# Kernel tuning notes

Hardware: AMD Instinct MI355X
Metric: run time of the kernel (lower is better)

The kernel has to match this reference:

```python
import jax, jax.numpy as jnp
import numpy as np

B = 262144
G = 21       # number of groups (hardcoded in the torch forward)
GS = 8       # features per group
BASIC = 13   # data[:, :13]
H = 512      # hidden_dim
OUT = 1      # output_size


def setup_inputs() -> dict:
    key = jax.random.key(0)
    k0, k1, k2, k3, k4, k5, k6 = jax.random.split(key, 7)
    data = jax.random.normal(k0, (B, BASIC + G * GS), dtype=jnp.float32)
    # per-group Linear(GS, 1): stacked weights [G, GS] and biases [G]
    gW = jax.random.normal(k1, (G, GS), dtype=jnp.float32) * 0.1
    gb = jax.random.normal(k2, (G,), dtype=jnp.float32) * 0.1
    W1 = jax.random.normal(k3, (BASIC + G, H), dtype=jnp.float32) * 0.1
    b1 = jax.random.normal(k4, (H,), dtype=jnp.float32) * 0.1
    W2 = jax.random.normal(k5, (H, OUT), dtype=jnp.float32) * 0.1
    b2 = jax.random.normal(k6, (OUT,), dtype=jnp.float32) * 0.1
    return {"data": data, "gW": gW, "gb": gb, "W1": W1, "b1": b1, "W2": W2, "b2": b2}


def reference(data, gW, gb, W1, b1, W2, b2):
    # Groups are the contiguous, exclusive column slices 13:181 -> [B, G, GS].
    grouped = data[:, BASIC:].reshape(data.shape[0], G, GS)
    # 21 tiny Linear(GS,1)+Sigmoid ops, fused into one batched contraction.
    gout = jax.nn.sigmoid(jnp.einsum("bgd,gd->bg", grouped, gW) + gb)  # [B, G]
    mixed = jnp.concatenate([data[:, :BASIC], gout], axis=1)           # [B, 13+21]
    h = jax.nn.relu(mixed @ W1 + b1)                                   # [B, H]
    return jax.nn.sigmoid(h @ W2 + b2)                                 # [B, OUT]
```

## Files before the change

### kernel.cpp

```cpp
#include <hip/hip_runtime.h>
#include <hip/hip_bf16.h>


#define B_ROWS 262144
#define DFEAT  181
#define BASICF 13
#define NG     21
#define MIXF   34
#define HID    512
#define NT     512
#define TILE   128
#define ROWS_PER_BLOCK 512
#define NTILES (ROWS_PER_BLOCK / TILE)
#define NBLK   (B_ROWS / ROWS_PER_BLOCK)

typedef __attribute__((ext_vector_type(8))) short short8;
typedef __attribute__((ext_vector_type(4))) float float4_t;

__device__ __forceinline__ short f2bf(float f) {
    union { float f; unsigned u; } v; v.f = f;
    unsigned r = (v.u + 0x7FFFu + ((v.u >> 16) & 1u)) >> 16;
    return (short)r;
}
__device__ __forceinline__ float sigm(float x) { return 1.0f / (1.0f + __expf(-x)); }

__global__ __launch_bounds__(NT, 4) void fused_mfma_kernel(
    const float* __restrict__ data, const float* __restrict__ gW,
    const float* __restrict__ gb, const float* __restrict__ W1,
    const float* __restrict__ b1, const float* __restrict__ W2,
    const float* __restrict__ b2, float* __restrict__ out)
{
    __shared__ __align__(16) short   W1f[32 * 64 * 8];
    __shared__ __align__(16) short   mixed[TILE * 32];
    __shared__ __align__(8)  float   mtail[TILE][2];
    __shared__ __align__(16) float4_t wbt[HID];
    __shared__ float gws[NG * 8];
    __shared__ float gbs[NG];

    const int tid = threadIdx.x;

    #pragma unroll 4
    for (int k = 0; k < 32; ++k) {
        int c = tid;
        int t = c >> 4, ci = c & 15;
        int l = ((k >> 3) << 4) + ci;
        int j = k & 7;
        W1f[(t * 64 + l) * 8 + j] = f2bf(W1[k * HID + c]);
    }
    {
        int c = tid;
        wbt[c] = (float4_t){ b1[c], W2[c], W1[32 * HID + c], W1[33 * HID + c] };
    }
    if (tid < NG * 8) gws[tid] = gW[tid];
    if (tid < NG)     gbs[tid] = gb[tid];
    __syncthreads();

    const int wave = tid >> 6;
    const int lane = tid & 63;
    const int lg   = lane >> 4;
    const int li   = lane & 15;
    const float b2v = b2[0];
    const int blk_row0 = blockIdx.x * ROWS_PER_BLOCK;

    {
        const int row0 = blk_row0;
        for (int it = 0; it < 9; ++it) {
            int u = tid + it * NT;
            if (u < TILE * MIXF) {
                int row = u / MIXF, c = u - row * MIXF;
                const float* dr = data + (size_t)(row0 + row) * DFEAT;
                if (c < BASICF) {
                    mixed[row * 32 + c] = f2bf(dr[c]);
                } else {
                    int g = c - BASICF;
                    const float* x = dr + BASICF + g * 8;
                    float s = gbs[g];
                    #pragma unroll
                    for (int k = 0; k < 8; ++k) s = fmaf(x[k], gws[g * 8 + k], s);
                    float v = sigm(s);
                    if (c < 32) mixed[row * 32 + c] = f2bf(v);
                    else        mtail[row][c - 32] = v;
                }
            }
        }
    }
    __syncthreads();

    for (int tile = 0; tile < NTILES; ++tile) {
        const int trow0 = blk_row0 + tile * TILE;

        short8 a0 = *(const short8*)&mixed[(wave * 16 + li) * 32 + lg * 8];
        float2 mt[4];
        #pragma unroll
        for (int j = 0; j < 4; ++j)
            mt[j] = *(const float2*)&mtail[wave * 16 + lg * 4 + j][0];
        __syncthreads();

        if (tile + 1 < NTILES) {
            const int row0 = trow0 + TILE;
            for (int it = 0; it < 9; ++it) {
                int u = tid + it * NT;
                if (u < TILE * MIXF) {
                    int row = u / MIXF, c = u - row * MIXF;
                    const float* dr = data + (size_t)(row0 + row) * DFEAT;
                    if (c < BASICF) {
                        mixed[row * 32 + c] = f2bf(dr[c]);
                    } else {
                        int g = c - BASICF;
                        const float* x = dr + BASICF + g * 8;
                        float s = gbs[g];
                        #pragma unroll
                        for (int k = 0; k < 8; ++k) s = fmaf(x[k], gws[g * 8 + k], s);
                        float v = sigm(s);
                        if (c < 32) mixed[row * 32 + c] = f2bf(v);
                        else        mtail[row][c - 32] = v;
                    }
                }
            }
        }

        float4_t acc = {0.f, 0.f, 0.f, 0.f};
        for (int t = 0; t < 32; ++t) {
            short8 bf = *(const short8*)&W1f[(t * 64 + lane) * 8];
            float4_t c4 = {0.f, 0.f, 0.f, 0.f};
            c4 = __builtin_amdgcn_mfma_f32_16x16x32_bf16(a0, bf, c4, 0, 0, 0);
            int c = t * 16 + li;
            float4_t wv = wbt[c];
            #pragma unroll
            for (int j = 0; j < 4; ++j) {
                float h = c4[j] + wv.x;
                h = fmaf(mt[j].x, wv.z, h);
                h = fmaf(mt[j].y, wv.w, h);
                h = fmaxf(h, 0.f);
                acc[j] = fmaf(h, wv.y, acc[j]);
            }
        }
        #pragma unroll
        for (int m = 1; m < 16; m <<= 1) {
            #pragma unroll
            for (int j = 0; j < 4; ++j) acc[j] += __shfl_xor(acc[j], m, 64);
        }
        if (li == 0) {
            #pragma unroll
            for (int j = 0; j < 4; ++j)
                out[trow0 + wave * 16 + lg * 4 + j] = sigm(acc[j] + b2v);
        }
        __syncthreads();
    }
}

extern "C" void kernel_launch(void* const* d_in, const int* in_sizes, int n_in,
                              void* d_out, int out_size, void* d_ws, size_t ws_size,
                              hipStream_t stream) {
    (void)in_sizes; (void)n_in; (void)out_size; (void)d_ws; (void)ws_size;
    const float* data = (const float*)d_in[0];
    const float* gW   = (const float*)d_in[1];
    const float* gb   = (const float*)d_in[2];
    const float* W1   = (const float*)d_in[3];
    const float* b1   = (const float*)d_in[4];
    const float* W2   = (const float*)d_in[5];
    const float* b2   = (const float*)d_in[6];
    float* out = (float*)d_out;
    fused_mfma_kernel<<<dim3(NBLK), dim3(NT), 0, stream>>>(data, gW, gb, W1, b1, W2, b2, out);
}
```

Before: 51.66 us.

## Restructure feature gathering into per-wave row loads with vectorized group dot products

Rebuilds the mixed-feature staging so each wave handles 16 rows, with lanes doing unaligned float4 loads of half a group and a shuffle to finish each 8-wide dot product. The group weights move from shared memory into registers, and the mixed LDS row stride is padded to 40. The aim is more coalesced global reads of the data rows, less index division, and fewer LDS bank conflicts. The tradeoff is that some lanes sit idle and the loads are unaligned. The launch-bounds occupancy hint is also dropped.

```diff
diff --git a/kernel.cpp b/kernel.cpp
--- a/kernel.cpp
+++ b/kernel.cpp
@@ -10,6 +10,7 @@
 #define HID    512
 #define NT     512
 #define TILE   128
+#define MSTRIDE 40
 #define ROWS_PER_BLOCK 512
 #define NTILES (ROWS_PER_BLOCK / TILE)
 #define NBLK   (B_ROWS / ROWS_PER_BLOCK)
@@ -24,24 +25,54 @@
 }
 __device__ __forceinline__ float sigm(float x) { return 1.0f / (1.0f + __expf(-x)); }
 
-__global__ __launch_bounds__(NT, 4) void fused_mfma_kernel(
+__device__ __forceinline__ float4_t load4u(const float* p) {
+    float4_t v;
+    __builtin_memcpy(&v, p, 16);
+    return v;
+}
+
+__device__ __forceinline__ void build_rows(
+    const float* __restrict__ data, int row0_global, int wave, int lane,
+    float4_t gwv, float gbv, short* __restrict__ mixed, float* __restrict__ mtail)
+{
+    #pragma unroll 4
+    for (int rr = 0; rr < 16; ++rr) {
+        const int row = wave * 16 + rr;
+        const float* dr = data + (size_t)(row0_global + row) * DFEAT;
+        if (lane < 42) {
+            float4_t x = load4u(dr + BASICF + lane * 4);
+            float p = fmaf(x[0], gwv[0],
+                      fmaf(x[1], gwv[1],
+                      fmaf(x[2], gwv[2], x[3] * gwv[3])));
+            p += __shfl_xor(p, 1, 64);
+            if ((lane & 1) == 0) {
+                int g = lane >> 1;
+                float v = sigm(p + gbv);
+                if (g < 19) mixed[row * MSTRIDE + BASICF + g] = f2bf(v);
+                else        mtail[row * 2 + (g - 19)] = v;
+            }
+        } else if (lane >= 43 && lane < 56) {
+            int c = lane - 43;
+            mixed[row * MSTRIDE + c] = f2bf(dr[c]);
+        }
+    }
+}
+
+__global__ __launch_bounds__(NT) void fused_mfma_kernel(
     const float* __restrict__ data, const float* __restrict__ gW,
     const float* __restrict__ gb, const float* __restrict__ W1,
     const float* __restrict__ b1, const float* __restrict__ W2,
     const float* __restrict__ b2, float* __restrict__ out)
 {
     __shared__ __align__(16) short   W1f[32 * 64 * 8];
-    __shared__ __align__(16) short   mixed[TILE * 32];
-    __shared__ __align__(8)  float   mtail[TILE][2];
     __shared__ __align__(16) float4_t wbt[HID];
-    __shared__ float gws[NG * 8];
-    __shared__ float gbs[NG];
+    __shared__ __align__(16) short   mixed[TILE * MSTRIDE];
+    __shared__ __align__(8)  float   mtail[TILE * 2];
 
     const int tid = threadIdx.x;
 
-    #pragma unroll 4
-    for (int k = 0; k < 32; ++k) {
-        int c = tid;
+    for (int idx = tid; idx < 32 * HID; idx += NT) {
+        int k = idx >> 9, c = idx & 511;
         int t = c >> 4, ci = c & 15;
         int l = ((k >> 3) << 4) + ci;
         int j = k & 7;
@@ -51,73 +82,37 @@
         int c = tid;
         wbt[c] = (float4_t){ b1[c], W2[c], W1[32 * HID + c], W1[33 * HID + c] };
     }
-    if (tid < NG * 8) gws[tid] = gW[tid];
-    if (tid < NG)     gbs[tid] = gb[tid];
-    __syncthreads();
 
     const int wave = tid >> 6;
     const int lane = tid & 63;
     const int lg   = lane >> 4;
     const int li   = lane & 15;
+
+    float4_t gwv = {0.f, 0.f, 0.f, 0.f};
+    float gbv = 0.f;
+    if (lane < 42) {
+        gwv = ((const float4_t*)gW)[lane];
+        gbv = gb[lane >> 1];
+    }
     const float b2v = b2[0];
     const int blk_row0 = blockIdx.x * ROWS_PER_BLOCK;
+    __syncthreads();
 
-    {
-        const int row0 = blk_row0;
-        for (int it = 0; it < 9; ++it) {
-            int u = tid + it * NT;
-            if (u < TILE * MIXF) {
-                int row = u / MIXF, c = u - row * MIXF;
-                const float* dr = data + (size_t)(row0 + row) * DFEAT;
-                if (c < BASICF) {
-                    mixed[row * 32 + c] = f2bf(dr[c]);
-                } else {
-                    int g = c - BASICF;
-                    const float* x = dr + BASICF + g * 8;
-                    float s = gbs[g];
-                    #pragma unroll
-                    for (int k = 0; k < 8; ++k) s = fmaf(x[k], gws[g * 8 + k], s);
-                    float v = sigm(s);
-                    if (c < 32) mixed[row * 32 + c] = f2bf(v);
-                    else        mtail[row][c - 32] = v;
-                }
-            }
-        }
-    }
+    build_rows(data, blk_row0, wave, lane, gwv, gbv, mixed, mtail);
     __syncthreads();
 
     for (int tile = 0; tile < NTILES; ++tile) {
         const int trow0 = blk_row0 + tile * TILE;
 
-        short8 a0 = *(const short8*)&mixed[(wave * 16 + li) * 32 + lg * 8];
+        short8 a0 = *(const short8*)&mixed[(wave * 16 + li) * MSTRIDE + lg * 8];
         float2 mt[4];
         #pragma unroll
         for (int j = 0; j < 4; ++j)
-            mt[j] = *(const float2*)&mtail[wave * 16 + lg * 4 + j][0];
+            mt[j] = *(const float2*)&mtail[(wave * 16 + lg * 4 + j) * 2];
         __syncthreads();
 
-        if (tile + 1 < NTILES) {
-            const int row0 = trow0 + TILE;
-            for (int it = 0; it < 9; ++it) {
-                int u = tid + it * NT;
-                if (u < TILE * MIXF) {
-                    int row = u / MIXF, c = u - row * MIXF;
-                    const float* dr = data + (size_t)(row0 + row) * DFEAT;
-                    if (c < BASICF) {
-                        mixed[row * 32 + c] = f2bf(dr[c]);
-                    } else {
-                        int g = c - BASICF;
-                        const float* x = dr + BASICF + g * 8;
-                        float s = gbs[g];
-                        #pragma unroll
-                        for (int k = 0; k < 8; ++k) s = fmaf(x[k], gws[g * 8 + k], s);
-                        float v = sigm(s);
-                        if (c < 32) mixed[row * 32 + c] = f2bf(v);
-                        else        mtail[row][c - 32] = v;
-                    }
-                }
-            }
-        }
+        if (tile + 1 < NTILES)
+            build_rows(data, trow0 + TILE, wave, lane, gwv, gbv, mixed, mtail);
 
         float4_t acc = {0.f, 0.f, 0.f, 0.f};
         for (int t = 0; t < 32; ++t) {
```

Result: slower. 76.45 us (+48.0%).
